# Optimization experiments

Hardware: AMD Instinct MI355X
Metric: run time of the kernel (lower is better)

## Reference

```python
import jax, jax.numpy as jnp
import numpy as np

EPS = 1e-5  # torch nn.LayerNorm default eps


def _layernorm(x, gamma, beta):
    mu = jnp.mean(x, axis=-1, keepdims=True)
    var = jnp.mean(jnp.square(x - mu), axis=-1, keepdims=True)
    return (x - mu) * jax.lax.rsqrt(var + EPS) * gamma + beta


def _swish(x):
    return x * jax.nn.sigmoid(x)


def setup_inputs() -> dict:
    key = jax.random.key(0)
    k0, k1, k2 = jax.random.split(key, 3)
    B, S, D = 8, 8192, 768
    H = D // 2  # 384
    x = jax.random.normal(k0, (B, S, D), dtype=jnp.float32)
    # kaiming_normal on Linear weight of shape [out, in]: std = sqrt(2/fan_in)
    W1 = jax.random.normal(k1, (H, D), dtype=jnp.float32) * np.sqrt(2.0 / D)
    W2 = jax.random.normal(k2, (D, H), dtype=jnp.float32) * np.sqrt(2.0 / H)
    ln1_g = jnp.ones((D,), jnp.float32)
    ln1_b = jnp.zeros((D,), jnp.float32)
    ln2_g = jnp.ones((H,), jnp.float32)
    ln2_b = jnp.zeros((H,), jnp.float32)
    return {"x": x, "W1": W1, "W2": W2, "ln1_g": ln1_g, "ln1_b": ln1_b,
            "ln2_g": ln2_g, "ln2_b": ln2_b}


def reference(x, W1, W2, ln1_g, ln1_b, ln2_g, ln2_b):
    # Block 1: LN(768) -> (dropout, inference no-op) -> Linear 768->384 (no bias) -> Swish
    h = _layernorm(x, ln1_g, ln1_b)
    h = jnp.einsum('bsd,hd->bsh', h, W1)
    h = _swish(h)
    # Block 2: LN(384) -> Linear 384->768 (no bias) -> Swish
    h = _layernorm(h, ln2_g, ln2_b)
    h = jnp.einsum('bsh,dh->bsd', h, W2)
    h = _swish(h)
    # Residual add
    return h + x
```

## Files before the change

### kernel.cpp

```cpp
#include <hip/hip_runtime.h>
#include <stdint.h>


typedef float  f32x4  __attribute__((ext_vector_type(4)));
typedef short  bf16x8 __attribute__((ext_vector_type(8)));

#define D1 768
#define H1 384

__device__ __forceinline__ unsigned short f32_to_bf16(float f) {
    union { float f; unsigned int u; } v; v.f = f;
    unsigned int u = v.u;
    return (unsigned short)((u + 0x7FFFu + ((u >> 16) & 1u)) >> 16);
}

__device__ __forceinline__ bf16x8 pack8(const float4& a, const float4& b) {
    union { bf16x8 v; unsigned short s[8]; } u;
    u.s[0] = f32_to_bf16(a.x); u.s[1] = f32_to_bf16(a.y);
    u.s[2] = f32_to_bf16(a.z); u.s[3] = f32_to_bf16(a.w);
    u.s[4] = f32_to_bf16(b.x); u.s[5] = f32_to_bf16(b.y);
    u.s[6] = f32_to_bf16(b.z); u.s[7] = f32_to_bf16(b.w);
    return u.v;
}

__global__ void prep_kernel(const float* __restrict__ W1, const float* __restrict__ W2,
                            const float* __restrict__ g1, const float* __restrict__ b1,
                            const float* __restrict__ g2, const float* __restrict__ b2,
                            unsigned short* __restrict__ W1g, unsigned short* __restrict__ W2g,
                            float* __restrict__ Gw1, float* __restrict__ Cb1,
                            float* __restrict__ Gw2, float* __restrict__ Cb2) {
    int wid  = (blockIdx.x * blockDim.x + threadIdx.x) >> 6;
    int lane = threadIdx.x & 63;
    if (wid < H1) {
        int r = wid;
        float sg = 0.f, sb = 0.f;
        for (int c = lane; c < D1; c += 64) {
            float w = W1[r * D1 + c];
            float g = g1[c], b = b1[c];
            sg += g * w; sb += b * w;
            W1g[r * D1 + c] = f32_to_bf16(w * g);
        }
        for (int off = 32; off; off >>= 1) { sg += __shfl_xor(sg, off); sb += __shfl_xor(sb, off); }
        if (lane == 0) { Gw1[r] = sg; Cb1[r] = sb; }
    } else if (wid < H1 + D1) {
        int r = wid - H1;
        float sg = 0.f, sb = 0.f;
        for (int c = lane; c < H1; c += 64) {
            float w = W2[r * H1 + c];
            float g = g2[c], b = b2[c];
            sg += g * w; sb += b * w;
            W2g[r * H1 + c] = f32_to_bf16(w * g);
        }
        for (int off = 32; off; off >>= 1) { sg += __shfl_xor(sg, off); sb += __shfl_xor(sb, off); }
        if (lane == 0) { Gw2[r] = sg; Cb2[r] = sb; }
    }
}

__global__ __launch_bounds__(256, 3) void fused_kernel(
    const float* __restrict__ x,
    const unsigned short* __restrict__ W1g, const unsigned short* __restrict__ W2g,
    const float* __restrict__ Gw1, const float* __restrict__ Cb1,
    const float* __restrict__ Gw2, const float* __restrict__ Cb2,
    float* __restrict__ out)
{
    __shared__ __align__(16) unsigned short ldsA[2][32 * 64];
    __shared__ __align__(16) unsigned short ldsS[32 * 384];
    __shared__ float red[4][32][2];
    __shared__ float stats1[32][2];
    __shared__ float stats2[32][2];

    const int tid  = threadIdx.x;
    const int wave = tid >> 6;
    const int lane = tid & 63;
    const int l15  = lane & 15;
    const int l4   = lane >> 4;
    const int row0 = blockIdx.x * 32;
    const int nb   = wave * 96;

    const int srow = tid >> 3;
    const int scol = (tid & 7) * 8;
    const float* xrow = x + (size_t)(row0 + srow) * D1 + scol;
    const int wb = ((srow * 128 + scol * 2) ^ ((srow & 7) << 4));

    f32x4 acc[2][6];
    #pragma unroll
    for (int m = 0; m < 2; ++m)
        #pragma unroll
        for (int n = 0; n < 6; ++n) acc[m][n] = f32x4{0.f, 0.f, 0.f, 0.f};

    float sum = 0.f, sumsq = 0.f;

    const unsigned short* w1p = W1g + (size_t)(nb + l15) * D1 + l4 * 8;

    {
        float4 v0 = *(const float4*)(xrow + 0);
        float4 v1 = *(const float4*)(xrow + 4);
        sum   += (v0.x + v0.y + v0.z + v0.w) + (v1.x + v1.y + v1.z + v1.w);
        sumsq += v0.x*v0.x + v0.y*v0.y + v0.z*v0.z + v0.w*v0.w
               + v1.x*v1.x + v1.y*v1.y + v1.z*v1.z + v1.w*v1.w;
        *(bf16x8*)((char*)ldsA[0] + wb) = pack8(v0, v1);
    }
    __syncthreads();

    int cur = 0;
    for (int kc = 0; kc < D1; kc += 64) {
        const bool hasNext = (kc + 64) < D1;
        float4 nv0, nv1;
        if (hasNext) {
            nv0 = *(const float4*)(xrow + kc + 64);
            nv1 = *(const float4*)(xrow + kc + 68);
        }
        const char* bufc = (const char*)ldsA[cur];
        #pragma unroll
        for (int ks = 0; ks < 2; ++ks) {
            bf16x8 bfr[6];
            #pragma unroll
            for (int nt = 0; nt < 6; ++nt)
                bfr[nt] = *(const bf16x8*)(w1p + nt * 16 * D1 + kc + ks * 32);
            bf16x8 afr[2];
            #pragma unroll
            for (int mt = 0; mt < 2; ++mt) {
                int row = mt * 16 + l15;
                int off = (row * 128 + ks * 64 + l4 * 16) ^ ((row & 7) << 4);
                afr[mt] = *(const bf16x8*)(bufc + off);
            }
            #pragma unroll
            for (int mt = 0; mt < 2; ++mt)
                #pragma unroll
                for (int nt = 0; nt < 6; ++nt)
                    acc[mt][nt] = __builtin_amdgcn_mfma_f32_16x16x32_bf16(
                        afr[mt], bfr[nt], acc[mt][nt], 0, 0, 0);
        }
        if (hasNext) {
            sum   += (nv0.x + nv0.y + nv0.z + nv0.w) + (nv1.x + nv1.y + nv1.z + nv1.w);
            sumsq += nv0.x*nv0.x + nv0.y*nv0.y + nv0.z*nv0.z + nv0.w*nv0.w
                   + nv1.x*nv1.x + nv1.y*nv1.y + nv1.z*nv1.z + nv1.w*nv1.w;
            *(bf16x8*)((char*)ldsA[cur ^ 1] + wb) = pack8(nv0, nv1);
        }
        __syncthreads();
        cur ^= 1;
    }

    sum   += __shfl_xor(sum,   1); sum   += __shfl_xor(sum,   2); sum   += __shfl_xor(sum,   4);
    sumsq += __shfl_xor(sumsq, 1); sumsq += __shfl_xor(sumsq, 2); sumsq += __shfl_xor(sumsq, 4);
    if ((tid & 7) == 0) {
        float mu  = sum * (1.f / 768.f);
        float var = sumsq * (1.f / 768.f) - mu * mu;
        stats1[srow][0] = mu;
        stats1[srow][1] = rsqrtf(var + 1e-5f);
    }
    __syncthreads();

    float gw1[6], cb1[6];
    #pragma unroll
    for (int nt = 0; nt < 6; ++nt) {
        int c = nb + nt * 16 + l15;
        gw1[nt] = Gw1[c]; cb1[nt] = Cb1[c];
    }

    #pragma unroll
    for (int mt = 0; mt < 2; ++mt) {
        #pragma unroll
        for (int reg = 0; reg < 4; ++reg) {
            int lrow = mt * 16 + l4 * 4 + reg;
            float mu = stats1[lrow][0], rs = stats1[lrow][1];
            float psum = 0.f, psq = 0.f;
            #pragma unroll
            for (int nt = 0; nt < 6; ++nt) {
                float h0 = acc[mt][nt][reg];
                float h  = rs * (h0 - mu * gw1[nt]) + cb1[nt];
                float s  = h / (1.f + __expf(-h));
                psum += s; psq += s * s;
                int col = nb + nt * 16 + l15;
                int byt = lrow * 768 + col * 2;
                *(unsigned short*)((char*)ldsS + (byt ^ ((lrow & 7) << 4))) = f32_to_bf16(s);
            }
            psum += __shfl_xor(psum, 1); psum += __shfl_xor(psum, 2);
            psum += __shfl_xor(psum, 4); psum += __shfl_xor(psum, 8);
            psq  += __shfl_xor(psq,  1); psq  += __shfl_xor(psq,  2);
            psq  += __shfl_xor(psq,  4); psq  += __shfl_xor(psq,  8);
            if (l15 == 0) { red[wave][lrow][0] = psum;
                            red[wave][lrow][1] = psq; }
        }
    }
    __syncthreads();
    if (tid < 32) {
        float s0 = 0.f, q0 = 0.f;
        #pragma unroll
        for (int w = 0; w < 4; ++w) { s0 += red[w][tid][0]; q0 += red[w][tid][1]; }
        float mu  = s0 * (1.f / 384.f);
        float var = q0 * (1.f / 384.f) - mu * mu;
        stats2[tid][0] = mu;
        stats2[tid][1] = rsqrtf(var + 1e-5f);
    }
    __syncthreads();

    #pragma unroll
    for (int p = 0; p < 2; ++p) {
        #pragma unroll
        for (int m = 0; m < 2; ++m)
            #pragma unroll
            for (int n = 0; n < 6; ++n) acc[m][n] = f32x4{0.f, 0.f, 0.f, 0.f};

        const int ncb = p * 384 + nb;
        const unsigned short* w2p = W2g + (size_t)(ncb + l15) * H1 + l4 * 8;

        #pragma unroll
        for (int ks2 = 0; ks2 < 12; ++ks2) {
            bf16x8 bcur[6];
            #pragma unroll
            for (int nt = 0; nt < 6; ++nt)
                bcur[nt] = *(const bf16x8*)(w2p + nt * 16 * H1 + ks2 * 32);
            bf16x8 afr[2];
            #pragma unroll
            for (int mt = 0; mt < 2; ++mt) {
                int row = mt * 16 + l15;
                int off = (row * 768 + ks2 * 64 + l4 * 16) ^ ((row & 7) << 4);
                afr[mt] = *(const bf16x8*)((const char*)ldsS + off);
            }
            #pragma unroll
            for (int mt = 0; mt < 2; ++mt)
                #pragma unroll
                for (int nt = 0; nt < 6; ++nt)
                    acc[mt][nt] = __builtin_amdgcn_mfma_f32_16x16x32_bf16(
                        afr[mt], bcur[nt], acc[mt][nt], 0, 0, 0);
        }

        float gw2[6], cb2[6];
        #pragma unroll
        for (int nt = 0; nt < 6; ++nt) {
            int c = ncb + nt * 16 + l15;
            gw2[nt] = Gw2[c]; cb2[nt] = Cb2[c];
        }
        #pragma unroll
        for (int mt = 0; mt < 2; ++mt) {
            #pragma unroll
            for (int reg = 0; reg < 4; ++reg) {
                int lrow = mt * 16 + l4 * 4 + reg;
                float mu2 = stats2[lrow][0], rs2 = stats2[lrow][1];
                #pragma unroll
                for (int nt = 0; nt < 6; ++nt) {
                    int col = ncb + nt * 16 + l15;
                    float y0 = acc[mt][nt][reg];
                    float y  = rs2 * (y0 - mu2 * gw2[nt]) + cb2[nt];
                    float o  = y / (1.f + __expf(-y));
                    size_t gi = (size_t)(row0 + lrow) * D1 + col;
                    out[gi] = o + x[gi];
                }
            }
        }
    }
}

extern "C" void kernel_launch(void* const* d_in, const int* in_sizes, int n_in,
                              void* d_out, int out_size, void* d_ws, size_t ws_size,
                              hipStream_t stream) {
    const float* x  = (const float*)d_in[0];
    const float* W1 = (const float*)d_in[1];
    const float* W2 = (const float*)d_in[2];
    const float* g1 = (const float*)d_in[3];
    const float* b1 = (const float*)d_in[4];
    const float* g2 = (const float*)d_in[5];
    const float* b2 = (const float*)d_in[6];
    float* out = (float*)d_out;

    char* ws = (char*)d_ws;
    unsigned short* W1g = (unsigned short*)(ws + 0);
    unsigned short* W2g = (unsigned short*)(ws + 589824);
    float* Gw1 = (float*)(ws + 1179648);
    float* Cb1 = (float*)(ws + 1181184);
    float* Gw2 = (float*)(ws + 1182720);
    float* Cb2 = (float*)(ws + 1185792);

    prep_kernel<<<288, 256, 0, stream>>>(W1, W2, g1, b1, g2, b2,
                                         W1g, W2g, Gw1, Cb1, Gw2, Cb2);
    fused_kernel<<<2048, 256, 0, stream>>>(x, W1g, W2g, Gw1, Cb1, Gw2, Cb2, out);
}
```

Baseline: 368.2 us.

## Load x A-fragments directly into registers per wave, dropping LDS staging

```diff
diff --git a/kernel.cpp b/kernel.cpp
--- a/kernel.cpp
+++ b/kernel.cpp
@@ -63,10 +63,8 @@
     const float* __restrict__ Gw2, const float* __restrict__ Cb2,
     float* __restrict__ out)
 {
-    __shared__ __align__(16) unsigned short ldsA[2][32 * 64];
     __shared__ __align__(16) unsigned short ldsS[32 * 384];
     __shared__ float red[4][32][2];
-    __shared__ float stats1[32][2];
     __shared__ float stats2[32][2];
 
     const int tid  = threadIdx.x;
@@ -77,79 +75,55 @@
     const int row0 = blockIdx.x * 32;
     const int nb   = wave * 96;
 
-    const int srow = tid >> 3;
-    const int scol = (tid & 7) * 8;
-    const float* xrow = x + (size_t)(row0 + srow) * D1 + scol;
-    const int wb = ((srow * 128 + scol * 2) ^ ((srow & 7) << 4));
-
     f32x4 acc[2][6];
     #pragma unroll
     for (int m = 0; m < 2; ++m)
         #pragma unroll
         for (int n = 0; n < 6; ++n) acc[m][n] = f32x4{0.f, 0.f, 0.f, 0.f};
 
-    float sum = 0.f, sumsq = 0.f;
+    float sum[2] = {0.f, 0.f}, sq[2] = {0.f, 0.f};
 
     const unsigned short* w1p = W1g + (size_t)(nb + l15) * D1 + l4 * 8;
-
-    {
-        float4 v0 = *(const float4*)(xrow + 0);
-        float4 v1 = *(const float4*)(xrow + 4);
-        sum   += (v0.x + v0.y + v0.z + v0.w) + (v1.x + v1.y + v1.z + v1.w);
-        sumsq += v0.x*v0.x + v0.y*v0.y + v0.z*v0.z + v0.w*v0.w
-               + v1.x*v1.x + v1.y*v1.y + v1.z*v1.z + v1.w*v1.w;
-        *(bf16x8*)((char*)ldsA[0] + wb) = pack8(v0, v1);
-    }
-    __syncthreads();
-
-    int cur = 0;
-    for (int kc = 0; kc < D1; kc += 64) {
-        const bool hasNext = (kc + 64) < D1;
-        float4 nv0, nv1;
-        if (hasNext) {
-            nv0 = *(const float4*)(xrow + kc + 64);
-            nv1 = *(const float4*)(xrow + kc + 68);
-        }
-        const char* bufc = (const char*)ldsA[cur];
+    const float* xA = x + (size_t)(row0 + l15) * D1 + l4 * 8;
+
+    for (int kc = 0; kc < 12; ++kc) {
+        bf16x8 afr[2][2];
+        #pragma unroll
+        for (int mt = 0; mt < 2; ++mt) {
+            const float* p = xA + mt * 16 * D1 + kc * 64;
+            float4 u0 = *(const float4*)(p + 0);
+            float4 u1 = *(const float4*)(p + 4);
+            float4 u2 = *(const float4*)(p + 32);
+            float4 u3 = *(const float4*)(p + 36);
+            sum[mt] += (u0.x+u0.y+u0.z+u0.w) + (u1.x+u1.y+u1.z+u1.w)
+                     + (u2.x+u2.y+u2.z+u2.w) + (u3.x+u3.y+u3.z+u3.w);
+            sq[mt]  += u0.x*u0.x+u0.y*u0.y+u0.z*u0.z+u0.w*u0.w
+                     + u1.x*u1.x+u1.y*u1.y+u1.z*u1.z+u1.w*u1.w
+                     + u2.x*u2.x+u2.y*u2.y+u2.z*u2.z+u2.w*u2.w
+                     + u3.x*u3.x+u3.y*u3.y+u3.z*u3.z+u3.w*u3.w;
+            afr[mt][0] = pack8(u0, u1);
+            afr[mt][1] = pack8(u2, u3);
+        }
         #pragma unroll
         for (int ks = 0; ks < 2; ++ks) {
             bf16x8 bfr[6];
             #pragma unroll
             for (int nt = 0; nt < 6; ++nt)
-                bfr[nt] = *(const bf16x8*)(w1p + nt * 16 * D1 + kc + ks * 32);
-            bf16x8 afr[2];
-            #pragma unroll
-            for (int mt = 0; mt < 2; ++mt) {
-                int row = mt * 16 + l15;
-                int off = (row * 128 + ks * 64 + l4 * 16) ^ ((row & 7) << 4);
-                afr[mt] = *(const bf16x8*)(bufc + off);
-            }
+                bfr[nt] = *(const bf16x8*)(w1p + nt * 16 * D1 + kc * 64 + ks * 32);
             #pragma unroll
             for (int mt = 0; mt < 2; ++mt)
                 #pragma unroll
                 for (int nt = 0; nt < 6; ++nt)
                     acc[mt][nt] = __builtin_amdgcn_mfma_f32_16x16x32_bf16(
-                        afr[mt], bfr[nt], acc[mt][nt], 0, 0, 0);
-        }
-        if (hasNext) {
-            sum   += (nv0.x + nv0.y + nv0.z + nv0.w) + (nv1.x + nv1.y + nv1.z + nv1.w);
-            sumsq += nv0.x*nv0.x + nv0.y*nv0.y + nv0.z*nv0.z + nv0.w*nv0.w
-                   + nv1.x*nv1.x + nv1.y*nv1.y + nv1.z*nv1.z + nv1.w*nv1.w;
-            *(bf16x8*)((char*)ldsA[cur ^ 1] + wb) = pack8(nv0, nv1);
-        }
-        __syncthreads();
-        cur ^= 1;
-    }
-
-    sum   += __shfl_xor(sum,   1); sum   += __shfl_xor(sum,   2); sum   += __shfl_xor(sum,   4);
-    sumsq += __shfl_xor(sumsq, 1); sumsq += __shfl_xor(sumsq, 2); sumsq += __shfl_xor(sumsq, 4);
-    if ((tid & 7) == 0) {
-        float mu  = sum * (1.f / 768.f);
-        float var = sumsq * (1.f / 768.f) - mu * mu;
-        stats1[srow][0] = mu;
-        stats1[srow][1] = rsqrtf(var + 1e-5f);
-    }
-    __syncthreads();
+                        afr[mt][ks], bfr[nt], acc[mt][nt], 0, 0, 0);
+        }
+    }
+
+    #pragma unroll
+    for (int mt = 0; mt < 2; ++mt) {
+        sum[mt] += __shfl_xor(sum[mt], 16); sum[mt] += __shfl_xor(sum[mt], 32);
+        sq[mt]  += __shfl_xor(sq[mt],  16); sq[mt]  += __shfl_xor(sq[mt],  32);
+    }
 
     float gw1[6], cb1[6];
     #pragma unroll
@@ -163,7 +137,9 @@
         #pragma unroll
         for (int reg = 0; reg < 4; ++reg) {
             int lrow = mt * 16 + l4 * 4 + reg;
-            float mu = stats1[lrow][0], rs = stats1[lrow][1];
+            float mu = __shfl(sum[mt], l4 * 4 + reg) * (1.f / 768.f);
+            float m2 = __shfl(sq[mt],  l4 * 4 + reg) * (1.f / 768.f);
+            float rs = rsqrtf(m2 - mu * mu + 1e-5f);
             float psum = 0.f, psq = 0.f;
             #pragma unroll
             for (int nt = 0; nt < 6; ++nt) {
```

New measurement: 426.7 us. 15.9% more time.
